# Performance work log

Hardware: AMD Instinct MI355X
Metric: run time of the kernel (lower is better)

## Reference

```python
import jax, jax.numpy as jnp
import numpy as np

L, H = 3, 8
B, N, D, E = 4, 256, 128, 128
NH, EH1, EH2 = 512, 512, 512


def _ln(x, g, b):
    m = x.mean(-1, keepdims=True)
    v = ((x - m) ** 2).mean(-1, keepdims=True)
    return (x - m) * jax.lax.rsqrt(v + 1e-5) * g + b


def setup_inputs() -> dict:
    key = jax.random.key(0)
    ks = jax.random.split(key, 16)
    w = lambda k, *s: jax.random.normal(k, s, jnp.float32) * 0.02
    inp = {
        'node_features': jax.random.normal(ks[0], (B, N, D), jnp.float32),
        'edge_features': jax.random.normal(ks[1], (B, N, N, E), jnp.float32),
        'Wqkv_n': w(ks[2], L, D, 3 * D), 'bqkv_n': jnp.zeros((L, 3 * D)),
        'Wqkv_e': w(ks[3], L, E, 3 * D), 'bqkv_e': jnp.zeros((L, 3 * D)),
        'Wo': w(ks[4], L, D, D), 'bo': jnp.zeros((L, D)),
        'Wn1': w(ks[5], L, D, NH), 'bn1': jnp.zeros((L, NH)),
        'Wn2': w(ks[6], L, NH, D), 'bn2': jnp.zeros((L, D)),
        'ln1n_g': jnp.ones((L, D)), 'ln1n_b': jnp.zeros((L, D)),
        'ln2n_g': jnp.ones((L, D)), 'ln2n_b': jnp.zeros((L, D)),
        'We1a': w(ks[7], L, 2 * D + 2 * E, EH1), 'be1a': jnp.zeros((L, EH1)),
        'We1b': w(ks[8], L, EH1, E), 'be1b': jnp.zeros((L, E)),
        'We2a': w(ks[9], L, E, EH2), 'be2a': jnp.zeros((L, EH2)),
        'We2b': w(ks[10], L, EH2, E), 'be2b': jnp.zeros((L, E)),
        'ln1e_g': jnp.ones((L, E)), 'ln1e_b': jnp.zeros((L, E)),
        'ln2e_g': jnp.ones((L, E)), 'ln2e_b': jnp.zeros((L, E)),
    }
    return inp


def reference(node_features, edge_features, Wqkv_n, bqkv_n, Wqkv_e, bqkv_e, Wo, bo,
              Wn1, bn1, Wn2, bn2, ln1n_g, ln1n_b, ln2n_g, ln2n_b,
              We1a, be1a, We1b, be1b, We2a, be2a, We2b, be2b,
              ln1e_g, ln1e_b, ln2e_g, ln2e_b):
    n, e = node_features, edge_features
    b_, N_, D_ = n.shape
    hd = D_ // H
    scale = 1.0 / np.sqrt(hd).astype(np.float32)
    for l in range(Wqkv_n.shape[0]):
        # ---- edge-biased attention ----
        qkv_n = (n @ Wqkv_n[l] + bqkv_n[l]).reshape(b_, N_, H, 3 * hd).transpose(0, 2, 1, 3)  # B,H,N,3hd
        q_n, k_n, v_n = jnp.split(qkv_n, 3, axis=-1)
        qkv_e = (e @ Wqkv_e[l] + bqkv_e[l]).reshape(b_, N_, N_, H, 3 * hd).transpose(0, 3, 1, 2, 4)  # B,H,N,N,3hd
        q_e, k_e, v_e = jnp.split(qkv_e, 3, axis=-1)
        q = q_n[:, :, :, None, :] + q_e  # B,H,N,N,hd
        # NOTE: the original torch code overwrites k with q (`k = q.reshape(...)`),
        # so scores are the squared norm of q; k_n/k_e are dead code. Faithful.
        scores = jnp.einsum('bhijd,bhijd->bhij', q, q) * scale
        att = jax.nn.softmax(scores, axis=-1)
        v = v_n[:, :, None, :, :] + v_e  # B,H,N,N,hd
        out = jnp.einsum('bhij,bhijd->bhid', att, v)  # B,H,N,hd
        out = out.transpose(0, 2, 1, 3).reshape(b_, N_, D_) @ Wo[l] + bo[l]
        n = _ln(n + out, ln1n_g[l], ln1n_b[l])
        ff = jax.nn.relu(n @ Wn1[l] + bn1[l]) @ Wn2[l] + bn2[l]
        n = _ln(n + ff, ln2n_g[l], ln2n_b[l])
        # ---- edge update ----
        src = jnp.broadcast_to(n[:, None, :, :], (b_, N_, N_, D_))  # node j
        tgt = jnp.broadcast_to(n[:, :, None, :], (b_, N_, N_, D_))  # node i
        cat = jnp.concatenate([e, e.transpose(0, 2, 1, 3), src, tgt], axis=-1)
        e1 = jax.nn.relu(cat @ We1a[l] + be1a[l]) @ We1b[l] + be1b[l]
        e = _ln(e + e1, ln1e_g[l], ln1e_b[l])
        e2 = jax.nn.relu(e @ We2a[l] + be2a[l]) @ We2b[l] + be2b[l]
        e = _ln(e + e2, ln2e_g[l], ln2e_b[l])
    return n
```

## Files before the change

### kernel.cpp

```cpp
#include <hip/hip_runtime.h>

typedef unsigned short u16;
typedef __bf16 bf16x8 __attribute__((ext_vector_type(8)));
typedef float f32x4 __attribute__((ext_vector_type(4)));

#define NB 4
#define NN 256
#define DD 128
#define RNN 262144

__device__ __forceinline__ u16 f2b(float f) {
    unsigned u = __builtin_bit_cast(unsigned, f);
    unsigned rb = ((u >> 16) & 1u) + 0x7FFFu;
    return (u16)((u + rb) >> 16);
}
__device__ __forceinline__ float b2f(u16 u) {
    return __builtin_bit_cast(float, ((unsigned)u) << 16);
}

__device__ __forceinline__ void glds16(const void* g, void* l) {
    __builtin_amdgcn_global_load_lds((const __attribute__((address_space(1))) void*)g,
                                     (__attribute__((address_space(3))) void*)l, 16, 0, 0);
}

__global__ void prep_weights(const float* __restrict__ Wqkv_e, const float* __restrict__ bqkv_e,
                             const float* __restrict__ We1a, const float* __restrict__ We1b,
                             const float* __restrict__ We2a, const float* __restrict__ We2b,
                             u16* wqT, u16* wv, float* bqp, float* bvp,
                             u16* w1f_e1, u16* w2f_e1, u16* w1f_e2, u16* w2f_e2) {
    int l = blockIdx.z, sec = blockIdx.y;
    int idx = blockIdx.x * 256 + threadIdx.x;
    if (sec == 0) {
        if (idx < 16384) {
            int n = idx >> 7, k = idx & 127;
            int col = (n >> 4) * 48 + (n & 15);
            wqT[l * 16384 + n * 128 + k] = f2b(Wqkv_e[l * 49152 + k * 384 + col]);
        }
    } else if (sec == 1) {
        if (idx < 16384) {
            int k = idx >> 7, c = idx & 127;
            int col = (c >> 4) * 48 + 32 + (c & 15);
            wv[l * 16384 + k * 128 + c] = f2b(Wqkv_e[l * 49152 + k * 384 + col]);
        }
        if (idx < 128) {
            bqp[l * 128 + idx] = bqkv_e[l * 384 + (idx >> 4) * 48 + (idx & 15)];
            bvp[l * 128 + idx] = bqkv_e[l * 384 + (idx >> 4) * 48 + 32 + (idx & 15)];
        }
    } else if (sec == 2) {
        if (idx < 131072) {
            int step = idx >> 13, q = step >> 2, kt = step & 3;
            int rem = idx & 8191;
            int nb = rem >> 10, ks = (rem >> 9) & 1, ln = (rem >> 3) & 63, j = rem & 7;
            int n = q * 128 + nb * 16 + (ln & 15);
            int k = kt * 64 + ks * 32 + (ln >> 4) * 8 + j;
            w1f_e1[l * 131072 + idx] = f2b(We1a[l * 262144 + k * 512 + n]);
        }
    } else if (sec == 3) {
        if (idx < 65536) {
            int step = idx >> 13, q = step >> 1, kt2 = step & 1;
            int rem = idx & 8191;
            int cb = rem >> 10, ks = (rem >> 9) & 1, ln = (rem >> 3) & 63, j = rem & 7;
            int c = cb * 16 + (ln & 15);
            int k = q * 128 + kt2 * 64 + ks * 32 + (ln >> 4) * 8 + j;
            w2f_e1[l * 65536 + idx] = f2b(We1b[l * 65536 + k * 128 + c]);
        }
    } else if (sec == 4) {
        if (idx < 65536) {
            int step = idx >> 13, q = step >> 1, kt = step & 1;
            int rem = idx & 8191;
            int nb = rem >> 10, ks = (rem >> 9) & 1, ln = (rem >> 3) & 63, j = rem & 7;
            int n = q * 128 + nb * 16 + (ln & 15);
            int k = kt * 64 + ks * 32 + (ln >> 4) * 8 + j;
            w1f_e2[l * 65536 + idx] = f2b(We2a[l * 65536 + k * 512 + n]);
        }
    } else {
        if (idx < 65536) {
            int step = idx >> 13, q = step >> 1, kt2 = step & 1;
            int rem = idx & 8191;
            int cb = rem >> 10, ks = (rem >> 9) & 1, ln = (rem >> 3) & 63, j = rem & 7;
            int c = cb * 16 + (ln & 15);
            int k = q * 128 + kt2 * 64 + ks * 32 + (ln >> 4) * 8 + j;
            w2f_e2[l * 65536 + idx] = f2b(We2b[l * 65536 + k * 128 + c]);
        }
    }
}

__global__ void init_e(const float4* __restrict__ src, ushort4* __restrict__ dst) {
    const long n4 = 8388608;
    for (long i = (long)blockIdx.x * blockDim.x + threadIdx.x; i < n4; i += (long)gridDim.x * blockDim.x) {
        float4 v = src[i];
        ushort4 o;
        o.x = f2b(v.x); o.y = f2b(v.y); o.z = f2b(v.z); o.w = f2b(v.w);
        dst[i] = o;
    }
}

__global__ void init_n(const float* __restrict__ node, float* __restrict__ nf) {
    int i = blockIdx.x * 256 + threadIdx.x;
    if (i < 131072) nf[i] = node[i];
}

__launch_bounds__(512)
__global__ void pre_node_kernel(const float* __restrict__ nf, const float* __restrict__ We1a,
                                float* __restrict__ preS, float* __restrict__ preT) {
    __shared__ float nr[128];
    int tid = threadIdx.x;
    int row = blockIdx.x;
    if (tid < 128) nr[tid] = nf[(long)row * 128 + tid];
    __syncthreads();
    int c = tid;
    float s = 0.f, t = 0.f;
    const float* Ws = We1a + (long)256 * 512 + c;
    const float* Wt = We1a + (long)384 * 512 + c;
    #pragma unroll 8
    for (int k = 0; k < 128; ++k) {
        float nv = nr[k];
        s += nv * Ws[k * 512];
        t += nv * Wt[k * 512];
    }
    preS[(long)row * 512 + c] = s;
    preT[(long)row * 512 + c] = t;
}

__global__ void qkvn_kernel(const float* __restrict__ nf, const float* __restrict__ W,
                            const float* __restrict__ bias, float* __restrict__ qn, float* __restrict__ vn) {
    __shared__ float nr[128];
    int tid = threadIdx.x;
    int row = blockIdx.x;
    if (tid < 128) nr[tid] = nf[(long)row * 128 + tid];
    __syncthreads();
    int c = tid & 127;
    bool isq = tid < 128;
    int col = (c >> 4) * 48 + (c & 15) + (isq ? 0 : 32);
    float a = bias[col];
    #pragma unroll 8
    for (int k = 0; k < 128; ++k) a += nr[k] * W[k * 384 + col];
    if (isq) qn[(long)row * 128 + c] = a;
    else     vn[(long)row * 128 + c] = a;
}

__launch_bounds__(256, 2)
__global__ void scores_kernel(const u16* __restrict__ ein, const u16* __restrict__ WqT,
                              const float* __restrict__ bqp, const float* __restrict__ qn,
                              float* __restrict__ scoresp) {
    __shared__ u16 As[128 * 64];
    __shared__ u16 Bs[128 * 64];
    int tid = threadIdx.x;
    int wid = tid >> 6, lane = tid & 63;
    int bid = blockIdx.x;
    int jhalf = bid & 1, bi = bid >> 1;
    int b = bi >> 8, i = bi & 255;
    int wr = wid >> 1, wc = wid & 1;

    f32x4 acc[4][4];
    f32x4 z = {0.f, 0.f, 0.f, 0.f};
    #pragma unroll
    for (int m = 0; m < 4; ++m)
        #pragma unroll
        for (int n = 0; n < 4; ++n) acc[m][n] = z;

    const long arow0 = ((long)(b * NN + i) * NN + jhalf * 128);
    for (int kt = 0; kt < 2; ++kt) {
        int k0 = kt << 6;
        #pragma unroll
        for (int p = 0; p < 4; ++p) {
            int r = p * 32 + (tid >> 3);
            int ch = tid & 7;
            const u16* src = ein + (arow0 + r) * 128 + k0 + ((ch ^ (r & 7)) << 3);
            glds16(src, (char*)As + (p << 12) + (wid << 10));
            int n = p * 32 + (tid >> 3);
            const u16* bsrc = WqT + (long)n * 128 + k0 + ((ch ^ (n & 7)) << 3);
            glds16(bsrc, (char*)Bs + (p << 12) + (wid << 10));
        }
        __syncthreads();
        #pragma unroll
        for (int ks = 0; ks < 2; ++ks) {
            bf16x8 af[4], bfr[4];
            #pragma unroll
            for (int m = 0; m < 4; ++m) {
                int r = wr * 64 + m * 16 + (lane & 15);
                int ch = (ks * 4 + (lane >> 4)) ^ (r & 7);
                af[m] = *reinterpret_cast<const bf16x8*>(&As[r * 64 + ch * 8]);
            }
            #pragma unroll
            for (int n = 0; n < 4; ++n) {
                int c = wc * 64 + n * 16 + (lane & 15);
                int ch = (ks * 4 + (lane >> 4)) ^ (c & 7);
                bfr[n] = *reinterpret_cast<const bf16x8*>(&Bs[c * 64 + ch * 8]);
            }
            #pragma unroll
            for (int m = 0; m < 4; ++m)
                #pragma unroll
                for (int n = 0; n < 4; ++n)
                    acc[m][n] = __builtin_amdgcn_mfma_f32_16x16x32_bf16(af[m], bfr[n], acc[m][n], 0, 0, 0);
        }
        __syncthreads();
    }
    const float* qnb = qn + (long)(b * NN + i) * 128;
    #pragma unroll
    for (int m = 0; m < 4; ++m) {
        #pragma unroll
        for (int n = 0; n < 4; ++n) {
            int col = wc * 64 + n * 16 + (lane & 15);
            float add = bqp[col] + qnb[col];
            float sv[4];
            #pragma unroll
            for (int t = 0; t < 4; ++t) { float qv = acc[m][n][t] + add; sv[t] = qv * qv; }
            #pragma unroll
            for (int mk = 1; mk <= 8; mk <<= 1)
                #pragma unroll
                for (int t = 0; t < 4; ++t) sv[t] += __shfl_xor(sv[t], mk);
            if ((lane & 15) == 0) {
                int head = wc * 4 + n;
                int jb = jhalf * 128 + wr * 64 + m * 16 + ((lane >> 4) << 2);
                long sbase = ((long)(b * 8 + head) * 256 + i) * 256 + jb;
                #pragma unroll
                for (int t = 0; t < 4; ++t) scoresp[sbase + t] = sv[t] * 0.25f;
            }
        }
    }
}

__launch_bounds__(256)
__global__ void attn_pv_kernel(const float* __restrict__ scoresp, const u16* __restrict__ ein,
                               const float* __restrict__ vn, const u16* __restrict__ Wv,
                               const float* __restrict__ bvp, float* __restrict__ attn_o) {
    __shared__ float s_s[8 * 256];
    __shared__ float g_s[8 * 128];
    __shared__ float part[256];
    int tid = threadIdx.x;
    int b = blockIdx.x >> 8, i = blockIdx.x & 255;
    for (int v = tid; v < 2048; v += 256) {
        int h = v >> 8, j = v & 255;
        s_s[v] = scoresp[((long)(b * 8 + h) * 256 + i) * 256 + j];
    }
    __syncthreads();
    {
        int h = tid >> 5, lg = tid & 31;
        float vals[8], mx = -1e30f;
        #pragma unroll
        for (int t = 0; t < 8; ++t) { vals[t] = s_s[h * 256 + lg + t * 32]; mx = fmaxf(mx, vals[t]); }
        #pragma unroll
        for (int mk = 16; mk; mk >>= 1) mx = fmaxf(mx, __shfl_xor(mx, mk));
        float sum = 0.f;
        #pragma unroll
        for (int t = 0; t < 8; ++t) { vals[t] = __expf(vals[t] - mx); sum += vals[t]; }
        #pragma unroll
        for (int mk = 16; mk; mk >>= 1) sum += __shfl_xor(sum, mk);
        float inv = 1.f / sum;
        #pragma unroll
        for (int t = 0; t < 8; ++t) s_s[h * 256 + lg + t * 32] = vals[t] * inv;
    }
    __syncthreads();
    {
        int k = tid & 127, h0 = tid >> 7;
        const u16* erow = ein + ((long)(b * NN + i) * NN) * 128 + k;
        float a0 = 0, a1 = 0, a2 = 0, a3 = 0;
        for (int j = 0; j < 256; ++j) {
            float ev = b2f(erow[(long)j * 128]);
            a0 += s_s[(h0    ) * 256 + j] * ev;
            a1 += s_s[(h0 + 2) * 256 + j] * ev;
            a2 += s_s[(h0 + 4) * 256 + j] * ev;
            a3 += s_s[(h0 + 6) * 256 + j] * ev;
        }
        g_s[(h0    ) * 128 + k] = a0;
        g_s[(h0 + 2) * 128 + k] = a1;
        g_s[(h0 + 4) * 128 + k] = a2;
        g_s[(h0 + 6) * 128 + k] = a3;
    }
    __syncthreads();
    {
        int c = tid & 127, half = tid >> 7;
        int h = c >> 4;
        float a = 0.f;
        for (int j = half * 128; j < half * 128 + 128; ++j)
            a += s_s[h * 256 + j] * vn[((long)(b * NN + j)) * 128 + c];
        for (int k = half * 64; k < half * 64 + 64; ++k)
            a += g_s[h * 128 + k] * b2f(Wv[k * 128 + c]);
        part[tid] = a;
    }
    __syncthreads();
    if (tid < 128)
        attn_o[((long)(b * NN + i)) * 128 + tid] = part[tid] + part[128 + tid] + bvp[tid];
}

__launch_bounds__(256)
__global__ void node_kernel(const float* __restrict__ attn_o, float* __restrict__ nf,
                            const float* __restrict__ Wo, const float* __restrict__ bo,
                            const float* __restrict__ Wn1, const float* __restrict__ bn1,
                            const float* __restrict__ Wn2, const float* __restrict__ bn2,
                            const float* __restrict__ g1, const float* __restrict__ b1,
                            const float* __restrict__ g2, const float* __restrict__ b2) {
    __shared__ float ao[128], nr[128], n1[128], hb[512];
    __shared__ float red[8];
    int tid = threadIdx.x;
    int wid = tid >> 6, lane = tid & 63;
    long base = (long)blockIdx.x * 128;
    if (tid < 128) { ao[tid] = attn_o[base + tid]; nr[tid] = nf[base + tid]; }
    __syncthreads();
    float x = 0.f;
    if (tid < 128) {
        float a = bo[tid];
        #pragma unroll 8
        for (int k = 0; k < 128; ++k) a += ao[k] * Wo[k * 128 + tid];
        x = nr[tid] + a;
    }
    float s = (tid < 128) ? x : 0.f, q = (tid < 128) ? x * x : 0.f;
    #pragma unroll
    for (int mk = 1; mk <= 32; mk <<= 1) { s += __shfl_xor(s, mk); q += __shfl_xor(q, mk); }
    if (lane == 0) { red[wid * 2] = s; red[wid * 2 + 1] = q; }
    __syncthreads();
    float sum = red[0] + red[2] + red[4] + red[6];
    float sq  = red[1] + red[3] + red[5] + red[7];
    float mean = sum * (1.f / 128.f);
    float var = sq * (1.f / 128.f) - mean * mean;
    float rs = rsqrtf(var + 1e-5f);
    __syncthreads();
    if (tid < 128) n1[tid] = (x - mean) * rs * g1[tid] + b1[tid];
    __syncthreads();
    for (int c = tid; c < 512; c += 256) {
        float a = bn1[c];
        #pragma unroll 8
        for (int k = 0; k < 128; ++k) a += n1[k] * Wn1[k * 512 + c];
        hb[c] = a > 0.f ? a : 0.f;
    }
    __syncthreads();
    float y = 0.f;
    if (tid < 128) {
        float a = bn2[tid];
        #pragma unroll 8
        for (int k = 0; k < 512; ++k) a += hb[k] * Wn2[k * 128 + tid];
        y = n1[tid] + a;
    }
    float s2 = (tid < 128) ? y : 0.f, q2 = (tid < 128) ? y * y : 0.f;
    #pragma unroll
    for (int mk = 1; mk <= 32; mk <<= 1) { s2 += __shfl_xor(s2, mk); q2 += __shfl_xor(q2, mk); }
    if (lane == 0) { red[wid * 2] = s2; red[wid * 2 + 1] = q2; }
    __syncthreads();
    sum = red[0] + red[2] + red[4] + red[6];
    sq  = red[1] + red[3] + red[5] + red[7];
    mean = sum * (1.f / 128.f);
    var = sq * (1.f / 128.f) - mean * mean;
    rs = rsqrtf(var + 1e-5f);
    if (tid < 128) {
        float o = (y - mean) * rs * g2[tid] + b2[tid];
        nf[base + tid] = o;
    }
}

template<int KT1, int CAT>
__launch_bounds__(256, 3)
__global__ void fused_mlp5(const u16* __restrict__ W1F, const float* __restrict__ b1v,
                           const u16* __restrict__ W2F, const float* __restrict__ b2v,
                           const u16* __restrict__ ein, const u16* __restrict__ Aplain,
                           const float* __restrict__ preS, const float* __restrict__ preT,
                           const float* __restrict__ lng, const float* __restrict__ lnb,
                           u16* __restrict__ e_dst) {
    __shared__ __align__(16) u16 A_lds[KT1 * 4096];
    __shared__ __align__(16) u16 Hs[8192];
    __shared__ float psum[256], psq[256];

    constexpr int K1 = KT1 * 64;
    int tid = threadIdx.x;
    int wid = tid >> 6, lane = tid & 63;
    long row0 = (long)blockIdx.x * 64;
    int b = (int)(row0 >> 16);
    int rem0 = (int)(row0 & 65535);
    int i_ = rem0 >> 8, j0 = rem0 & 255;

    #pragma unroll
    for (int kt = 0; kt < KT1; ++kt)
        #pragma unroll
        for (int pp = 0; pp < 2; ++pp) {
            int r = pp * 32 + (tid >> 3);
            int ch = tid & 7;
            const u16* src;
            if constexpr (CAT) {
                long ridx = (kt < 2) ? (long)(b * NN + i_) * NN + (j0 + r)
                                     : (long)(b * NN + (j0 + r)) * NN + i_;
                src = ein + ridx * DD + ((kt & 1) << 6) + ((ch ^ (r & 7)) << 3);
            } else {
                src = Aplain + (row0 + r) * K1 + (kt << 6) + ((ch ^ (r & 7)) << 3);
            }
            glds16(src, (char*)A_lds + kt * 8192 + (pp << 12) + (wid << 10));
        }
    asm volatile("s_waitcnt vmcnt(0)" ::: "memory");
    __builtin_amdgcn_sched_barrier(0);
    __builtin_amdgcn_s_barrier();
    __builtin_amdgcn_sched_barrier(0);

    const u16* w1base = W1F + (wid * 2) * 1024 + lane * 8;
    const u16* w2base = W2F + (wid * 2) * 1024 + lane * 8;

    f32x4 z = {0.f, 0.f, 0.f, 0.f};
    f32x4 acc1[2][4], acc2[4][2];
    #pragma unroll
    for (int a = 0; a < 4; ++a) { acc2[a][0] = z; acc2[a][1] = z; }

    bf16x8 afA[4], afB[4], g2A[4], g2B[4];

    auto AFLD = [&](bf16x8 (&d)[4], int q, int kt) {
        const u16* p = w1base + ((q * KT1 + kt) << 13);
        d[0] = *reinterpret_cast<const bf16x8*>(p);
        d[1] = *reinterpret_cast<const bf16x8*>(p + 1024);
        d[2] = *reinterpret_cast<const bf16x8*>(p + 512);
        d[3] = *reinterpret_cast<const bf16x8*>(p + 1536);
    };
    auto BFLD = [&](bf16x8 (&d)[4], int q, int kt2) {
        const u16* p = w2base + ((q * 2 + kt2) << 13);
        d[0] = *reinterpret_cast<const bf16x8*>(p);
        d[1] = *reinterpret_cast<const bf16x8*>(p + 1024);
        d[2] = *reinterpret_cast<const bf16x8*>(p + 512);
        d[3] = *reinterpret_cast<const bf16x8*>(p + 1536);
    };
    auto G1K = [&](bf16x8 (&cur)[4], int kt) {
        #pragma unroll
        for (int ks = 0; ks < 2; ++ks) {
            bf16x8 bfr[4];
            #pragma unroll
            for (int rf = 0; rf < 4; ++rf) {
                int r = rf * 16 + (lane & 15);
                int ch = (ks * 4 + (lane >> 4)) ^ (r & 7);
                bfr[rf] = *reinterpret_cast<const bf16x8*>(&A_lds[kt * 4096 + r * 64 + ch * 8]);
            }
            #pragma unroll
            for (int mn = 0; mn < 2; ++mn)
                #pragma unroll
                for (int rf = 0; rf < 4; ++rf)
                    acc1[mn][rf] = __builtin_amdgcn_mfma_f32_16x16x32_bf16(cur[ks * 2 + mn], bfr[rf], acc1[mn][rf], 0, 0, 0);
        }
    };
    auto G2K = [&](bf16x8 (&w)[4], int kt2) {
        #pragma unroll
        for (int ks = 0; ks < 2; ++ks) {
            bf16x8 af2[4];
            #pragma unroll
            for (int rf = 0; rf < 4; ++rf) {
                int r = rf * 16 + (lane & 15);
                int c8 = kt2 * 8 + ks * 4 + (lane >> 4);
                int cs = (c8 & 8) | ((c8 ^ r) & 7);
                af2[rf] = *reinterpret_cast<const bf16x8*>((const char*)Hs + r * 256 + cs * 16);
            }
            #pragma unroll
            for (int rf = 0; rf < 4; ++rf)
                #pragma unroll
                for (int cf = 0; cf < 2; ++cf)
                    acc2[rf][cf] = __builtin_amdgcn_mfma_f32_16x16x32_bf16(af2[rf], w[ks * 2 + cf], acc2[rf][cf], 0, 0, 0);
        }
    };

    AFLD(afA, 0, 0);
    for (int q = 0; q < 4; ++q) {
        #pragma unroll
        for (int mn = 0; mn < 2; ++mn)
            #pragma unroll
            for (int rf = 0; rf < 4; ++rf) acc1[mn][rf] = z;

        if constexpr (KT1 == 4) {
            AFLD(afB, q, 1); G1K(afA, 0);
            AFLD(afA, q, 2); G1K(afB, 1);
            AFLD(afB, q, 3); G1K(afA, 2);
            G1K(afB, 3);
        } else {
            AFLD(afB, q, 1); G1K(afA, 0);
            G1K(afB, 1);
        }

        BFLD(g2A, q, 0);
        if (q) {
            __builtin_amdgcn_sched_barrier(0);
            __builtin_amdgcn_s_barrier();
            __builtin_amdgcn_sched_barrier(0);
        }
        #pragma unroll
        for (int mn = 0; mn < 2; ++mn) {
            int nl0 = wid * 32 + mn * 16 + ((lane >> 4) << 2);
            int n0g = (q << 7) + nl0;
            float4 bb = *reinterpret_cast<const float4*>(&b1v[n0g]);
            if constexpr (CAT) {
                float4 pt = *reinterpret_cast<const float4*>(&preT[(long)(b * NN + i_) * 512 + n0g]);
                bb.x += pt.x; bb.y += pt.y; bb.z += pt.z; bb.w += pt.w;
            }
            #pragma unroll
            for (int rf = 0; rf < 4; ++rf) {
                int r = rf * 16 + (lane & 15);
                float b0 = bb.x, b1_ = bb.y, b2_ = bb.z, b3 = bb.w;
                if constexpr (CAT) {
                    float4 ps = *reinterpret_cast<const float4*>(&preS[(long)(b * NN + j0 + r) * 512 + n0g]);
                    b0 += ps.x; b1_ += ps.y; b2_ += ps.z; b3 += ps.w;
                }
                float v0 = acc1[mn][rf][0] + b0; v0 = v0 > 0.f ? v0 : 0.f;
                float v1 = acc1[mn][rf][1] + b1_; v1 = v1 > 0.f ? v1 : 0.f;
                float v2 = acc1[mn][rf][2] + b2_; v2 = v2 > 0.f ? v2 : 0.f;
                float v3 = acc1[mn][rf][3] + b3; v3 = v3 > 0.f ? v3 : 0.f;
                uint2 pk;
                pk.x = (unsigned)f2b(v0) | ((unsigned)f2b(v1) << 16);
                pk.y = (unsigned)f2b(v2) | ((unsigned)f2b(v3) << 16);
                int c8 = nl0 >> 3;
                int cs = (c8 & 8) | ((c8 ^ r) & 7);
                *reinterpret_cast<uint2*>((char*)Hs + r * 256 + cs * 16 + (nl0 & 7) * 2) = pk;
            }
        }
        asm volatile("s_waitcnt lgkmcnt(0)" ::: "memory");
        __builtin_amdgcn_sched_barrier(0);
        __builtin_amdgcn_s_barrier();
        __builtin_amdgcn_sched_barrier(0);

        BFLD(g2B, q, 1);
        G2K(g2A, 0);
        if (q < 3) AFLD(afA, q + 1, 0);
        G2K(g2B, 1);
    }

    #pragma unroll
    for (int rf = 0; rf < 4; ++rf) {
        float sv[4] = {0.f, 0.f, 0.f, 0.f}, qv[4] = {0.f, 0.f, 0.f, 0.f};
        #pragma unroll
        for (int cf = 0; cf < 2; ++cf) {
            int c = wid * 32 + cf * 16 + (lane & 15);
            float bb = b2v[c];
            int kk = c & 63, kreg = c >> 6;
            #pragma unroll
            for (int t = 0; t < 4; ++t) {
                int r = rf * 16 + ((lane >> 4) << 2) + t;
                float er = b2f(A_lds[kreg * 4096 + r * 64 + (((kk >> 3) ^ (r & 7)) << 3) + (kk & 7)]);
                float x = acc2[rf][cf][t] + bb + er;
                acc2[rf][cf][t] = x;
                sv[t] += x;
                qv[t] += x * x;
            }
        }
        #pragma unroll
        for (int mk = 1; mk <= 8; mk <<= 1)
            #pragma unroll
            for (int t = 0; t < 4; ++t) { sv[t] += __shfl_xor(sv[t], mk); qv[t] += __shfl_xor(qv[t], mk); }
        if ((lane & 15) == 0) {
            #pragma unroll
            for (int t = 0; t < 4; ++t) {
                int r = rf * 16 + ((lane >> 4) << 2) + t;
                psum[r * 4 + wid] = sv[t];
                psq[r * 4 + wid] = qv[t];
            }
        }
    }
    __syncthreads();
    #pragma unroll
    for (int rf = 0; rf < 4; ++rf) {
        #pragma unroll
        for (int t = 0; t < 4; ++t) {
            int r = rf * 16 + ((lane >> 4) << 2) + t;
            float sum = psum[r * 4] + psum[r * 4 + 1] + psum[r * 4 + 2] + psum[r * 4 + 3];
            float sq  = psq[r * 4] + psq[r * 4 + 1] + psq[r * 4 + 2] + psq[r * 4 + 3];
            float mean = sum * (1.f / 128.f);
            float var = sq * (1.f / 128.f) - mean * mean;
            float rs = rsqrtf(var + 1e-5f);
            #pragma unroll
            for (int cf = 0; cf < 2; ++cf) {
                int c = wid * 32 + cf * 16 + (lane & 15);
                float o = (acc2[rf][cf][t] - mean) * rs * lng[c] + lnb[c];
                Hs[r * 128 + c] = f2b(o);
            }
        }
    }
    __syncthreads();
    #pragma unroll
    for (int pp = 0; pp < 4; ++pp) {
        ulonglong2 v = *reinterpret_cast<const ulonglong2*>((char*)Hs + (pp << 12) + tid * 16);
        *reinterpret_cast<ulonglong2*>((char*)e_dst + row0 * 256 + (pp << 12) + tid * 16) = v;
    }
}

extern "C" void kernel_launch(void* const* d_in, const int* in_sizes, int n_in,
                              void* d_out, int out_size, void* d_ws, size_t ws_size,
                              hipStream_t stream) {
    (void)in_sizes; (void)n_in; (void)out_size; (void)ws_size;
    const float* node   = (const float*)d_in[0];
    const float* edge   = (const float*)d_in[1];
    const float* Wqkv_n = (const float*)d_in[2];
    const float* bqkv_n = (const float*)d_in[3];
    const float* Wqkv_e = (const float*)d_in[4];
    const float* bqkv_e = (const float*)d_in[5];
    const float* Wo     = (const float*)d_in[6];
    const float* bo     = (const float*)d_in[7];
    const float* Wn1    = (const float*)d_in[8];
    const float* bn1    = (const float*)d_in[9];
    const float* Wn2    = (const float*)d_in[10];
    const float* bn2    = (const float*)d_in[11];
    const float* ln1n_g = (const float*)d_in[12];
    const float* ln1n_b = (const float*)d_in[13];
    const float* ln2n_g = (const float*)d_in[14];
    const float* ln2n_b = (const float*)d_in[15];
    const float* We1a   = (const float*)d_in[16];
    const float* be1a   = (const float*)d_in[17];
    const float* We1b   = (const float*)d_in[18];
    const float* be1b   = (const float*)d_in[19];
    const float* We2a   = (const float*)d_in[20];
    const float* be2a   = (const float*)d_in[21];
    const float* We2b   = (const float*)d_in[22];
    const float* be2b   = (const float*)d_in[23];
    const float* ln1e_g = (const float*)d_in[24];
    const float* ln1e_b = (const float*)d_in[25];
    const float* ln2e_g = (const float*)d_in[26];
    const float* ln2e_b = (const float*)d_in[27];

    size_t off = 0;
    char* wsb = (char*)d_ws;
    auto alloc = [&](size_t bytes) -> void* {
        void* p = wsb + off;
        off = (off + bytes + 255) & ~(size_t)255;
        return p;
    };
    u16* eb0      = (u16*)alloc((size_t)RNN * 128 * 2);
    u16* eb1      = (u16*)alloc((size_t)RNN * 128 * 2);
    float* scoresp= (float*)alloc((size_t)2097152 * 4);
    float* qn     = (float*)alloc(131072 * 4);
    float* vn     = (float*)alloc(131072 * 4);
    float* attn_o = (float*)alloc(131072 * 4);
    float* nf     = (float*)alloc(131072 * 4);
    float* preS   = (float*)alloc((size_t)1024 * 512 * 4);
    float* preT   = (float*)alloc((size_t)1024 * 512 * 4);
    u16* wqT      = (u16*)alloc(3 * 16384 * 2);
    u16* wv       = (u16*)alloc(3 * 16384 * 2);
    float* bqp    = (float*)alloc(3 * 128 * 4);
    float* bvp    = (float*)alloc(3 * 128 * 4);
    u16* w1f_e1   = (u16*)alloc(3 * 131072ull * 2);
    u16* w2f_e1   = (u16*)alloc(3 * 65536 * 2);
    u16* w1f_e2   = (u16*)alloc(3 * 65536 * 2);
    u16* w2f_e2   = (u16*)alloc(3 * 65536 * 2);

    {
        dim3 g(512, 6, 3);
        prep_weights<<<g, 256, 0, stream>>>(Wqkv_e, bqkv_e, We1a, We1b, We2a, We2b,
                                            wqT, wv, bqp, bvp, w1f_e1, w2f_e1, w1f_e2, w2f_e2);
    }
    init_e<<<2048, 256, 0, stream>>>((const float4*)edge, (ushort4*)eb0);
    init_n<<<512, 256, 0, stream>>>(node, nf);

    for (int l = 0; l < 3; ++l) {
        u16* ein  = (l & 1) ? eb1 : eb0;
        u16* eout = (l & 1) ? eb0 : eb1;
        qkvn_kernel<<<1024, 256, 0, stream>>>(nf, Wqkv_n + l * 49152, bqkv_n + l * 384, qn, vn);
        scores_kernel<<<2048, 256, 0, stream>>>(ein, wqT + l * 16384, bqp + l * 128, qn, scoresp);
        attn_pv_kernel<<<1024, 256, 0, stream>>>(scoresp, ein, vn, wv + l * 16384, bvp + l * 128, attn_o);
        node_kernel<<<1024, 256, 0, stream>>>(attn_o, nf,
                                              Wo + l * 16384, bo + l * 128,
                                              Wn1 + l * 65536, bn1 + l * 512,
                                              Wn2 + l * 65536, bn2 + l * 128,
                                              ln1n_g + l * 128, ln1n_b + l * 128,
                                              ln2n_g + l * 128, ln2n_b + l * 128);
        pre_node_kernel<<<1024, 512, 0, stream>>>(nf, We1a + (size_t)l * 262144, preS, preT);
        fused_mlp5<4, 1><<<4096, 256, 0, stream>>>(w1f_e1 + l * 131072, be1a + l * 512,
                                                   w2f_e1 + l * 65536, be1b + l * 128,
                                                   ein, nullptr, preS, preT,
                                                   ln1e_g + l * 128, ln1e_b + l * 128, eout);
        fused_mlp5<2, 0><<<4096, 256, 0, stream>>>(w1f_e2 + l * 65536, be2a + l * 512,
                                                   w2f_e2 + l * 65536, be2b + l * 128,
                                                   nullptr, eout, nullptr, nullptr,
                                                   ln2e_g + l * 128, ln2e_b + l * 128, eout);
    }
    hipMemcpyAsync(d_out, nf, 131072 * sizeof(float), hipMemcpyDeviceToDevice, stream);
}
```

Baseline: 1.322 ms.

## Fuse both edge MLP blocks into one kernel keeping tiles in LDS

Merges the two per-layer edge MLP kernels (concat MLP + LN, then second MLP + LN) into one kernel. The intermediate LayerNorm output stays in shared memory, stored in the A-tile region that is no longer needed, and feeds the second MLP directly. This removes a global write and read of the full edge tensor and one launch per layer. It also switches the bf16 conversion to the native cast, which adds work to an already register-heavy kernel and may change occupancy.

```diff
diff --git a/kernel.cpp b/kernel.cpp
--- a/kernel.cpp
+++ b/kernel.cpp
@@ -16,6 +16,15 @@
 }
 __device__ __forceinline__ float b2f(u16 u) {
     return __builtin_bit_cast(float, ((unsigned)u) << 16);
+}
+__device__ __forceinline__ u16 b16(float f) {
+    __bf16 h = (__bf16)f;
+    return __builtin_bit_cast(u16, h);
+}
+__device__ __forceinline__ unsigned pk2(float a, float b) {
+    ushort2 r;
+    r.x = b16(a); r.y = b16(b);
+    return __builtin_bit_cast(unsigned, r);
 }
 
 __device__ __forceinline__ void glds16(const void* g, void* l) {
@@ -348,19 +357,20 @@
     }
 }
 
-template<int KT1, int CAT>
 __launch_bounds__(256, 3)
-__global__ void fused_mlp5(const u16* __restrict__ W1F, const float* __restrict__ b1v,
-                           const u16* __restrict__ W2F, const float* __restrict__ b2v,
-                           const u16* __restrict__ ein, const u16* __restrict__ Aplain,
+__global__ void fused_mlp6(const u16* __restrict__ W1aF, const float* __restrict__ b1a,
+                           const u16* __restrict__ W1bF, const float* __restrict__ b1b,
+                           const u16* __restrict__ W2aF, const float* __restrict__ b2a,
+                           const u16* __restrict__ W2bF, const float* __restrict__ b2b,
+                           const u16* __restrict__ ein,
                            const float* __restrict__ preS, const float* __restrict__ preT,
-                           const float* __restrict__ lng, const float* __restrict__ lnb,
+                           const float* __restrict__ ln1g, const float* __restrict__ ln1b,
+                           const float* __restrict__ ln2g, const float* __restrict__ ln2b,
                            u16* __restrict__ e_dst) {
-    __shared__ __align__(16) u16 A_lds[KT1 * 4096];
+    __shared__ __align__(16) u16 A_lds[16384];
     __shared__ __align__(16) u16 Hs[8192];
     __shared__ float psum[256], psq[256];
 
-    constexpr int K1 = KT1 * 64;
     int tid = threadIdx.x;
     int wid = tid >> 6, lane = tid & 63;
     long row0 = (long)blockIdx.x * 64;
@@ -369,19 +379,14 @@
     int i_ = rem0 >> 8, j0 = rem0 & 255;
 
     #pragma unroll
-    for (int kt = 0; kt < KT1; ++kt)
+    for (int kt = 0; kt < 4; ++kt)
         #pragma unroll
         for (int pp = 0; pp < 2; ++pp) {
             int r = pp * 32 + (tid >> 3);
             int ch = tid & 7;
-            const u16* src;
-            if constexpr (CAT) {
-                long ridx = (kt < 2) ? (long)(b * NN + i_) * NN + (j0 + r)
-                                     : (long)(b * NN + (j0 + r)) * NN + i_;
-                src = ein + ridx * DD + ((kt & 1) << 6) + ((ch ^ (r & 7)) << 3);
-            } else {
-                src = Aplain + (row0 + r) * K1 + (kt << 6) + ((ch ^ (r & 7)) << 3);
-            }
+            long ridx = (kt < 2) ? (long)(b * NN + i_) * NN + (j0 + r)
+                                 : (long)(b * NN + (j0 + r)) * NN + i_;
+            const u16* src = ein + ridx * DD + ((kt & 1) << 6) + ((ch ^ (r & 7)) << 3);
             glds16(src, (char*)A_lds + kt * 8192 + (pp << 12) + (wid << 10));
         }
     asm volatile("s_waitcnt vmcnt(0)" ::: "memory");
@@ -389,31 +394,23 @@
     __builtin_amdgcn_s_barrier();
     __builtin_amdgcn_sched_barrier(0);
 
-    const u16* w1base = W1F + (wid * 2) * 1024 + lane * 8;
-    const u16* w2base = W2F + (wid * 2) * 1024 + lane * 8;
+    const u16* w1a = W1aF + (wid * 2) * 1024 + lane * 8;
+    const u16* w1b = W1bF + (wid * 2) * 1024 + lane * 8;
+    const u16* w2a = W2aF + (wid * 2) * 1024 + lane * 8;
+    const u16* w2b = W2bF + (wid * 2) * 1024 + lane * 8;
 
     f32x4 z = {0.f, 0.f, 0.f, 0.f};
     f32x4 acc1[2][4], acc2[4][2];
-    #pragma unroll
-    for (int a = 0; a < 4; ++a) { acc2[a][0] = z; acc2[a][1] = z; }
-
     bf16x8 afA[4], afB[4], g2A[4], g2B[4];
 
-    auto AFLD = [&](bf16x8 (&d)[4], int q, int kt) {
-        const u16* p = w1base + ((q * KT1 + kt) << 13);
+    auto FR4 = [&](bf16x8 (&d)[4], const u16* base, int step) {
+        const u16* p = base + (step << 13);
         d[0] = *reinterpret_cast<const bf16x8*>(p);
         d[1] = *reinterpret_cast<const bf16x8*>(p + 1024);
         d[2] = *reinterpret_cast<const bf16x8*>(p + 512);
         d[3] = *reinterpret_cast<const bf16x8*>(p + 1536);
     };
-    auto BFLD = [&](bf16x8 (&d)[4], int q, int kt2) {
-        const u16* p = w2base + ((q * 2 + kt2) << 13);
-        d[0] = *reinterpret_cast<const bf16x8*>(p);
-        d[1] = *reinterpret_cast<const bf16x8*>(p + 1024);
-        d[2] = *reinterpret_cast<const bf16x8*>(p + 512);
-        d[3] = *reinterpret_cast<const bf16x8*>(p + 1536);
-    };
-    auto G1K = [&](bf16x8 (&cur)[4], int kt) {
+    auto G1K = [&](bf16x8 (&cur)[4], int reg) {
         #pragma unroll
         for (int ks = 0; ks < 2; ++ks) {
             bf16x8 bfr[4];
@@ -421,7 +418,7 @@
             for (int rf = 0; rf < 4; ++rf) {
                 int r = rf * 16 + (lane & 15);
                 int ch = (ks * 4 + (lane >> 4)) ^ (r & 7);
-                bfr[rf] = *reinterpret_cast<const bf16x8*>(&A_lds[kt * 4096 + r * 64 + ch * 8]);
+                bfr[rf] = *reinterpret_cast<const bf16x8*>(&A_lds[reg * 4096 + r * 64 + ch * 8]);
             }
             #pragma unroll
             for (int mn = 0; mn < 2; ++mn)
@@ -448,36 +445,13 @@
                     acc2[rf][cf] = __builtin_amdgcn_mfma_f32_16x16x32_bf16(af2[rf], w[ks * 2 + cf], acc2[rf][cf], 0, 0, 0);
         }
     };
-
-    AFLD(afA, 0, 0);
-    for (int q = 0; q < 4; ++q) {
-        #pragma unroll
-        for (int mn = 0; mn < 2; ++mn)
-            #pragma unroll
-            for (int rf = 0; rf < 4; ++rf) acc1[mn][rf] = z;
-
-        if constexpr (KT1 == 4) {
-            AFLD(afB, q, 1); G1K(afA, 0);
-            AFLD(afA, q, 2); G1K(afB, 1);
-            AFLD(afB, q, 3); G1K(afA, 2);
-            G1K(afB, 3);
-        } else {
-            AFLD(afB, q, 1); G1K(afA, 0);
-            G1K(afB, 1);
-        }
-
-        BFLD(g2A, q, 0);
-        if (q) {
-            __builtin_amdgcn_sched_barrier(0);
-            __builtin_amdgcn_s_barrier();
-            __builtin_amdgcn_sched_barrier(0);
-        }
+    auto EPI = [&](int q, const float* bias, bool wp) {
         #pragma unroll
         for (int mn = 0; mn < 2; ++mn) {
             int nl0 = wid * 32 + mn * 16 + ((lane >> 4) << 2);
             int n0g = (q << 7) + nl0;
-            float4 bb = *reinterpret_cast<const float4*>(&b1v[n0g]);
-            if constexpr (CAT) {
+            float4 bb = *reinterpret_cast<const float4*>(&bias[n0g]);
+            if (wp) {
                 float4 pt = *reinterpret_cast<const float4*>(&preT[(long)(b * NN + i_) * 512 + n0g]);
                 bb.x += pt.x; bb.y += pt.y; bb.z += pt.z; bb.w += pt.w;
             }
@@ -485,7 +459,7 @@
             for (int rf = 0; rf < 4; ++rf) {
                 int r = rf * 16 + (lane & 15);
                 float b0 = bb.x, b1_ = bb.y, b2_ = bb.z, b3 = bb.w;
-                if constexpr (CAT) {
+                if (wp) {
                     float4 ps = *reinterpret_cast<const float4*>(&preS[(long)(b * NN + j0 + r) * 512 + n0g]);
                     b0 += ps.x; b1_ += ps.y; b2_ += ps.z; b3 += ps.w;
                 }
@@ -494,55 +468,78 @@
                 float v2 = acc1[mn][rf][2] + b2_; v2 = v2 > 0.f ? v2 : 0.f;
                 float v3 = acc1[mn][rf][3] + b3; v3 = v3 > 0.f ? v3 : 0.f;
                 uint2 pk;
-                pk.x = (unsigned)f2b(v0) | ((unsigned)f2b(v1) << 16);
-                pk.y = (unsigned)f2b(v2) | ((unsigned)f2b(v3) << 16);
+                pk.x = pk2(v0, v1);
+                pk.y = pk2(v2, v3);
                 int c8 = nl0 >> 3;
                 int cs = (c8 & 8) | ((c8 ^ r) & 7);
                 *reinterpret_cast<uint2*>((char*)Hs + r * 256 + cs * 16 + (nl0 & 7) * 2) = pk;
             }
         }
+    };
+    auto LNA = [&](const float* bias, int rb) {
+        #pragma unroll
+        for (int rf = 0; rf < 4; ++rf) {
+            float sv[4] = {0.f, 0.f, 0.f, 0.f}, qv[4] = {0.f, 0.f, 0.f, 0.f};
+            #pragma unroll
+            for (int cf = 0; cf < 2; ++cf) {
+                int c = wid * 32 + cf * 16 + (lane & 15);
+                float bb = bias[c];
+                int kk = c & 63, kreg = rb + (c >> 6);
+                #pragma unroll
+                for (int t = 0; t < 4; ++t) {
+                    int r = rf * 16 + ((lane >> 4) << 2) + t;
+                    float er = b2f(A_lds[kreg * 4096 + r * 64 + (((kk >> 3) ^ (r & 7)) << 3) + (kk & 7)]);
+                    float x = acc2[rf][cf][t] + bb + er;
+                    acc2[rf][cf][t] = x;
+                    sv[t] += x;
+                    qv[t] += x * x;
+                }
+            }
+            #pragma unroll
+            for (int mk = 1; mk <= 8; mk <<= 1)
+                #pragma unroll
+                for (int t = 0; t < 4; ++t) { sv[t] += __shfl_xor(sv[t], mk); qv[t] += __shfl_xor(qv[t], mk); }
+            if ((lane & 15) == 0) {
+                #pragma unroll
+                for (int t = 0; t < 4; ++t) {
+                    int r = rf * 16 + ((lane >> 4) << 2) + t;
+                    psum[r * 4 + wid] = sv[t];
+                    psq[r * 4 + wid] = qv[t];
+                }
+            }
+        }
+    };
+
+    #pragma unroll
+    for (int rf = 0; rf < 4; ++rf) { acc2[rf][0] = z; acc2[rf][1] = z; }
+    FR4(afA, w1a, 0);
+    for (int q = 0; q < 4; ++q) {
+        #pragma unroll
+        for (int mn = 0; mn < 2; ++mn)
+            #pragma unroll
+            for (int rf = 0; rf < 4; ++rf) acc1[mn][rf] = z;
+        FR4(afB, w1a, q * 4 + 1); G1K(afA, 0);
+        FR4(afA, w1a, q * 4 + 2); G1K(afB, 1);
+        FR4(afB, w1a, q * 4 + 3); G1K(afA, 2);
+        G1K(afB, 3);
+        FR4(g2A, w1b, q * 2 + 0);
+        if (q) {
+            __builtin_amdgcn_sched_barrier(0);
+            __builtin_amdgcn_s_barrier();
+            __builtin_amdgcn_sched_barrier(0);
+        }
+        EPI(q, b1a, true);
         asm volatile("s_waitcnt lgkmcnt(0)" ::: "memory");
         __builtin_amdgcn_sched_barrier(0);
         __builtin_amdgcn_s_barrier();
         __builtin_amdgcn_sched_barrier(0);
-
-        BFLD(g2B, q, 1);
+        FR4(g2B, w1b, q * 2 + 1);
         G2K(g2A, 0);
-        if (q < 3) AFLD(afA, q + 1, 0);
+        if (q < 3) FR4(afA, w1a, (q + 1) * 4);
         G2K(g2B, 1);
     }
 
-    #pragma unroll
-    for (int rf = 0; rf < 4; ++rf) {
-        float sv[4] = {0.f, 0.f, 0.f, 0.f}, qv[4] = {0.f, 0.f, 0.f, 0.f};
-        #pragma unroll
-        for (int cf = 0; cf < 2; ++cf) {
-            int c = wid * 32 + cf * 16 + (lane & 15);
-            float bb = b2v[c];
-            int kk = c & 63, kreg = c >> 6;
-            #pragma unroll
-            for (int t = 0; t < 4; ++t) {
-                int r = rf * 16 + ((lane >> 4) << 2) + t;
-                float er = b2f(A_lds[kreg * 4096 + r * 64 + (((kk >> 3) ^ (r & 7)) << 3) + (kk & 7)]);
-                float x = acc2[rf][cf][t] + bb + er;
-                acc2[rf][cf][t] = x;
-                sv[t] += x;
-                qv[t] += x * x;
-            }
-        }
-        #pragma unroll
-        for (int mk = 1; mk <= 8; mk <<= 1)
-            #pragma unroll
-            for (int t = 0; t < 4; ++t) { sv[t] += __shfl_xor(sv[t], mk); qv[t] += __shfl_xor(qv[t], mk); }
-        if ((lane & 15) == 0) {
-            #pragma unroll
-            for (int t = 0; t < 4; ++t) {
-                int r = rf * 16 + ((lane >> 4) << 2) + t;
-                psum[r * 4 + wid] = sv[t];
-                psq[r * 4 + wid] = qv[t];
-            }
-        }
-    }
+    LNA(b1b, 0);
     __syncthreads();
     #pragma unroll
     for (int rf = 0; rf < 4; ++rf) {
@@ -557,15 +554,65 @@
             #pragma unroll
             for (int cf = 0; cf < 2; ++cf) {
                 int c = wid * 32 + cf * 16 + (lane & 15);
-                float o = (acc2[rf][cf][t] - mean) * rs * lng[c] + lnb[c];
-                Hs[r * 128 + c] = f2b(o);
+                float o = (acc2[rf][cf][t] - mean) * rs * ln1g[c] + ln1b[c];
+                int kk = c & 63;
+                A_lds[(2 + (c >> 6)) * 4096 + r * 64 + (((kk >> 3) ^ (r & 7)) << 3) + (kk & 7)] = b16(o);
+            }
+        }
+    }
+    __syncthreads();
+
+    #pragma unroll
+    for (int rf = 0; rf < 4; ++rf) { acc2[rf][0] = z; acc2[rf][1] = z; }
+    FR4(afA, w2a, 0);
+    for (int q = 0; q < 4; ++q) {
+        #pragma unroll
+        for (int mn = 0; mn < 2; ++mn)
+            #pragma unroll
+            for (int rf = 0; rf < 4; ++rf) acc1[mn][rf] = z;
+        FR4(afB, w2a, q * 2 + 1); G1K(afA, 2);
+        G1K(afB, 3);
+        FR4(g2A, w2b, q * 2 + 0);
+        if (q) {
+            __builtin_amdgcn_sched_barrier(0);
+            __builtin_amdgcn_s_barrier();
+            __builtin_amdgcn_sched_barrier(0);
+        }
+        EPI(q, b2a, false);
+        asm volatile("s_waitcnt lgkmcnt(0)" ::: "memory");
+        __builtin_amdgcn_sched_barrier(0);
+        __builtin_amdgcn_s_barrier();
+        __builtin_amdgcn_sched_barrier(0);
+        FR4(g2B, w2b, q * 2 + 1);
+        G2K(g2A, 0);
+        if (q < 3) FR4(afA, w2a, (q + 1) * 2);
+        G2K(g2B, 1);
+    }
+
+    LNA(b2b, 2);
+    __syncthreads();
+    #pragma unroll
+    for (int rf = 0; rf < 4; ++rf) {
+        #pragma unroll
+        for (int t = 0; t < 4; ++t) {
+            int r = rf * 16 + ((lane >> 4) << 2) + t;
+            float sum = psum[r * 4] + psum[r * 4 + 1] + psum[r * 4 + 2] + psum[r * 4 + 3];
+            float sq  = psq[r * 4] + psq[r * 4 + 1] + psq[r * 4 + 2] + psq[r * 4 + 3];
+            float mean = sum * (1.f / 128.f);
+            float var = sq * (1.f / 128.f) - mean * mean;
+            float rs = rsqrtf(var + 1e-5f);
+            #pragma unroll
+            for (int cf = 0; cf < 2; ++cf) {
+                int c = wid * 32 + cf * 16 + (lane & 15);
+                float o = (acc2[rf][cf][t] - mean) * rs * ln2g[c] + ln2b[c];
+                A_lds[r * 128 + c] = b16(o);
             }
         }
     }
     __syncthreads();
     #pragma unroll
     for (int pp = 0; pp < 4; ++pp) {
-        ulonglong2 v = *reinterpret_cast<const ulonglong2*>((char*)Hs + (pp << 12) + tid * 16);
+        ulonglong2 v = *reinterpret_cast<const ulonglong2*>((char*)A_lds + (pp << 12) + tid * 16);
         *reinterpret_cast<ulonglong2*>((char*)e_dst + row0 * 256 + (pp << 12) + tid * 16) = v;
     }
 }
@@ -649,14 +696,14 @@
                                               ln1n_g + l * 128, ln1n_b + l * 128,
                                               ln2n_g + l * 128, ln2n_b + l * 128);
         pre_node_kernel<<<1024, 512, 0, stream>>>(nf, We1a + (size_t)l * 262144, preS, preT);
-        fused_mlp5<4, 1><<<4096, 256, 0, stream>>>(w1f_e1 + l * 131072, be1a + l * 512,
-                                                   w2f_e1 + l * 65536, be1b + l * 128,
-                                                   ein, nullptr, preS, preT,
-                                                   ln1e_g + l * 128, ln1e_b + l * 128, eout);
-        fused_mlp5<2, 0><<<4096, 256, 0, stream>>>(w1f_e2 + l * 65536, be2a + l * 512,
-                                                   w2f_e2 + l * 65536, be2b + l * 128,
-                                                   nullptr, eout, nullptr, nullptr,
-                                                   ln2e_g + l * 128, ln2e_b + l * 128, eout);
+        fused_mlp6<<<4096, 256, 0, stream>>>(w1f_e1 + l * 131072, be1a + l * 512,
+                                             w2f_e1 + l * 65536, be1b + l * 128,
+                                             w1f_e2 + l * 65536, be2a + l * 512,
+                                             w2f_e2 + l * 65536, be2b + l * 128,
+                                             ein, preS, preT,
+                                             ln1e_g + l * 128, ln1e_b + l * 128,
+                                             ln2e_g + l * 128, ln2e_b + l * 128,
+                                             eout);
     }
     hipMemcpyAsync(d_out, nf, 131072 * sizeof(float), hipMemcpyDeviceToDevice, stream);
 }
```

After: 1.304 ms, median of 2. No clear change (-1.4%).
